# Kernel tuning notes

Measured on AMD Instinct MI355X. Metric: run time of the kernel, lower is better.

## Reference

```python
import jax, jax.numpy as jnp
import numpy as np

B, T, H, F = 32, 2048, 1024, 1024  # batch, kv_len, hidden_size, feature_size


def setup_inputs() -> dict:
    key = jax.random.key(0)
    ks = jax.random.split(key, 6)
    s = 0.02  # param init scale
    return {
        "query": jax.random.normal(ks[0], (B, 1, H), jnp.float32),
        "keys": jax.random.normal(ks[1], (B, T, F), jnp.float32),
        "Wa_w": jax.random.normal(ks[2], (H, H), jnp.float32) * s,
        "Wa_b": jnp.zeros((H,), jnp.float32),
        "Ua_w": jax.random.normal(ks[3], (H, F), jnp.float32) * s,
        "Ua_b": jnp.zeros((H,), jnp.float32),
        "Va_w": jax.random.normal(ks[4], (1, H), jnp.float32) * s,
        "Va_b": jnp.zeros((1,), jnp.float32),
    }


def reference(query, keys, Wa_w, Wa_b, Ua_w, Ua_b, Va_w, Va_b):
    # Wa(query): [B,1,H]; Ua(keys): [B,T,H]
    q = jnp.einsum('bqh,oh->bqo', query, Wa_w) + Wa_b
    k = jnp.einsum('btf,of->bto', keys, Ua_w) + Ua_b
    e = jnp.tanh(q + k)                                   # [B,T,H] (broadcast over q dim of size 1)
    scores = jnp.einsum('bth,h->bt', e, Va_w[0]) + Va_b[0]  # Va(...).squeeze(2) -> [B,T]
    scores = scores[:, None, :]                           # unsqueeze(1) -> [B,1,T]
    weights = jax.nn.softmax(scores, axis=-1)             # [B,1,T]
    context = jnp.einsum('bqt,btf->bqf', weights, keys)   # bmm -> [B,1,F]
    return context, weights
```

## Files before the change

### kernel.cpp

```cpp
#include <hip/hip_runtime.h>
#include <hip/hip_bf16.h>

typedef float  f32x4 __attribute__((ext_vector_type(4)));
typedef short  s16x8 __attribute__((ext_vector_type(8)));
typedef __hip_bfloat16 bf16;

#define BDIM 32
#define TDIM 2048
#define HDIM 1024
#define FDIM 1024
#define MTOT (BDIM*TDIM)

#define GLOAD16(gp, lp) __builtin_amdgcn_global_load_lds(                     \
    (const __attribute__((address_space(1))) void*)(gp),                      \
    (__attribute__((address_space(3))) void*)(lp), 16, 0, 0)

__global__ __launch_bounds__(256) void cvt_bf16_kernel(
    const float* __restrict__ src, bf16* __restrict__ dst, int n8)
{
    int i = blockIdx.x * 256 + threadIdx.x;
    const int stride = gridDim.x * 256;
    for (; i < n8; i += stride) {
        const f32x4 a = ((const f32x4*)src)[2 * i];
        const f32x4 b = ((const f32x4*)src)[2 * i + 1];
        union { bf16 h[8]; s16x8 v; } u;
        #pragma unroll
        for (int j = 0; j < 4; ++j) {
            u.h[j]     = __float2bfloat16(a[j]);
            u.h[4 + j] = __float2bfloat16(b[j]);
        }
        ((s16x8*)dst)[i] = u.v;
    }
}

__global__ __launch_bounds__(256) void qeff_kernel(
    const float* __restrict__ query, const float* __restrict__ Wa_w,
    const float* __restrict__ Wa_b,  const float* __restrict__ Ua_b,
    float* __restrict__ qe)
{
    const int lane = threadIdx.x & 63;
    const int gw   = blockIdx.x * 4 + (threadIdx.x >> 6);
    const int b    = gw >> 10;
    const int o    = gw & 1023;
    const float* qp = query + (size_t)b * HDIM;
    const float* wp = Wa_w  + (size_t)o * HDIM;
    float s = 0.f;
    #pragma unroll
    for (int i = 0; i < 16; ++i) {
        const int h = i * 64 + lane;
        s += qp[h] * wp[h];
    }
    #pragma unroll
    for (int off = 32; off > 0; off >>= 1) s += __shfl_down(s, off);
    if (lane == 0) qe[gw] = s + Wa_b[o] + Ua_b[o];
}

#define STAGE_A(buf_, kb_, h_, s_) GLOAD16(                                    \
    Ab + (size_t)(M0 + (h_)*128 + (((s_)>>1)<<4) + srow) * FDIM               \
       + (kb_) + (((s_)&1)<<5) + scg*8,                                        \
    &As[buf_][((((h_)*8 + ((s_)>>1)) * 2 + ((s_)&1)) << 9)])
#define STAGE_B(buf_, kb_, h_, s_) GLOAD16(                                    \
    Bb + (size_t)(N0 + (h_)*128 + (((s_)>>1)<<4) + srow) * FDIM               \
       + (kb_) + (((s_)&1)<<5) + scg*8,                                        \
    &Bs[buf_][((((h_)*8 + ((s_)>>1)) * 2 + ((s_)&1)) << 9)])

__global__ __launch_bounds__(512, 2) void score_gemm_256_kernel(
    const bf16* __restrict__ Ab, const bf16* __restrict__ Bb,
    const float* __restrict__ qe, const float* __restrict__ Va,
    float* __restrict__ scores)
{
    __shared__ bf16 As[2][16384];
    __shared__ bf16 Bs[2][16384];

    const int tid  = threadIdx.x;
    const int lane = tid & 63;
    const int w    = tid >> 6;
    const int wr   = w >> 2;
    const int wc   = w & 3;

    const int bid   = blockIdx.x;
    const int local = bid >> 3;
    const int mt    = (bid & 7) * 32 + (local >> 2);
    const int nt    = local & 3;
    const int M0 = mt * 256, N0 = nt * 256;

    const int srow = lane >> 2;
    const int scg  = (lane & 3) ^ ((lane >> 4) & 3);
    const int r    = lane & 15;
    const int roff = r * 32 + (((lane >> 4) ^ ((r >> 2) & 3)) & 3) * 8;

    f32x4 acc[8][4];
    #pragma unroll
    for (int m = 0; m < 8; ++m)
        #pragma unroll
        for (int n = 0; n < 4; ++n) acc[m][n] = (f32x4){0.f, 0.f, 0.f, 0.f};

    STAGE_A(0, 0, 0, w); STAGE_A(0, 0, 0, w + 8);
    STAGE_A(0, 0, 1, w); STAGE_A(0, 0, 1, w + 8);
    STAGE_B(0, 0, 0, w); STAGE_B(0, 0, 0, w + 8);
    STAGE_B(0, 0, 1, w); STAGE_B(0, 0, 1, w + 8);
    asm volatile("s_waitcnt vmcnt(0)" ::: "memory");
    __builtin_amdgcn_s_barrier();

    for (int t = 0; t < 16; ++t) {
        const int rb  = t & 1, wbuf = rb ^ 1;
        const int kt1 = (t + 1) << 6;
        const bool pf = (t + 1 < 16);

        s16x8 a[4][2];
        s16x8 bq[4][2];

        #pragma unroll
        for (int mf = 0; mf < 4; ++mf)
            #pragma unroll
            for (int ks = 0; ks < 2; ++ks)
                a[mf][ks] = *(const s16x8*)
                    &As[rb][(((wr * 8 + mf) * 2 + ks) << 9) + roff];
        #pragma unroll
        for (int nf = 0; nf < 2; ++nf)
            #pragma unroll
            for (int ks = 0; ks < 2; ++ks)
                bq[nf][ks] = *(const s16x8*)
                    &Bs[rb][(((wc * 4 + nf) * 2 + ks) << 9) + roff];
        if (pf) {
            STAGE_A(wbuf, kt1, 0, w); STAGE_A(wbuf, kt1, 0, w + 8);
            STAGE_A(wbuf, kt1, 1, w); STAGE_A(wbuf, kt1, 1, w + 8);
        }
        __builtin_amdgcn_s_barrier();
        __builtin_amdgcn_s_setprio(1);
        #pragma unroll
        for (int mf = 0; mf < 4; ++mf)
            #pragma unroll
            for (int nf = 0; nf < 2; ++nf)
                #pragma unroll
                for (int ks = 0; ks < 2; ++ks)
                    acc[mf][nf] = __builtin_amdgcn_mfma_f32_16x16x32_bf16(
                        a[mf][ks], bq[nf][ks], acc[mf][nf], 0, 0, 0);
        __builtin_amdgcn_s_setprio(0);
        __builtin_amdgcn_s_barrier();

        #pragma unroll
        for (int nf = 2; nf < 4; ++nf)
            #pragma unroll
            for (int ks = 0; ks < 2; ++ks)
                bq[nf][ks] = *(const s16x8*)
                    &Bs[rb][(((wc * 4 + nf) * 2 + ks) << 9) + roff];
        if (pf) {
            STAGE_B(wbuf, kt1, 0, w); STAGE_B(wbuf, kt1, 0, w + 8);
            STAGE_B(wbuf, kt1, 1, w); STAGE_B(wbuf, kt1, 1, w + 8);
        }
        __builtin_amdgcn_s_barrier();
        __builtin_amdgcn_s_setprio(1);
        #pragma unroll
        for (int mf = 0; mf < 4; ++mf)
            #pragma unroll
            for (int nf = 2; nf < 4; ++nf)
                #pragma unroll
                for (int ks = 0; ks < 2; ++ks)
                    acc[mf][nf] = __builtin_amdgcn_mfma_f32_16x16x32_bf16(
                        a[mf][ks], bq[nf][ks], acc[mf][nf], 0, 0, 0);
        __builtin_amdgcn_s_setprio(0);
        __builtin_amdgcn_s_barrier();

        #pragma unroll
        for (int mf = 0; mf < 4; ++mf)
            #pragma unroll
            for (int ks = 0; ks < 2; ++ks)
                a[mf][ks] = *(const s16x8*)
                    &As[rb][(((wr * 8 + 4 + mf) * 2 + ks) << 9) + roff];
        __builtin_amdgcn_s_barrier();
        __builtin_amdgcn_s_setprio(1);
        #pragma unroll
        for (int mf = 0; mf < 4; ++mf)
            #pragma unroll
            for (int nf = 2; nf < 4; ++nf)
                #pragma unroll
                for (int ks = 0; ks < 2; ++ks)
                    acc[4 + mf][nf] = __builtin_amdgcn_mfma_f32_16x16x32_bf16(
                        a[mf][ks], bq[nf][ks], acc[4 + mf][nf], 0, 0, 0);
        __builtin_amdgcn_s_setprio(0);
        __builtin_amdgcn_s_barrier();

        __builtin_amdgcn_s_setprio(1);
        #pragma unroll
        for (int mf = 0; mf < 4; ++mf)
            #pragma unroll
            for (int nf = 0; nf < 2; ++nf)
                #pragma unroll
                for (int ks = 0; ks < 2; ++ks)
                    acc[4 + mf][nf] = __builtin_amdgcn_mfma_f32_16x16x32_bf16(
                        a[mf][ks], bq[nf][ks], acc[4 + mf][nf], 0, 0, 0);
        __builtin_amdgcn_s_setprio(0);
        asm volatile("s_waitcnt vmcnt(0)" ::: "memory");
        __builtin_amdgcn_s_barrier();
        __builtin_amdgcn_sched_barrier(0);
    }

    const int b = M0 >> 11;
    const float* qrow = qe + (size_t)b * HDIM;
    #pragma unroll
    for (int mf = 0; mf < 8; ++mf) {
        float part[4] = {0.f, 0.f, 0.f, 0.f};
        #pragma unroll
        for (int nf = 0; nf < 4; ++nf) {
            const int c    = N0 + wc * 64 + nf * 16 + (lane & 15);
            const float va = Va[c];
            const float qv = qrow[c];
            #pragma unroll
            for (int j = 0; j < 4; ++j) {
                const float x = qv + acc[mf][nf][j];
                const float e = __expf(2.0f * x);
                part[j] += va * (1.0f - 2.0f / (e + 1.0f));
            }
        }
        #pragma unroll
        for (int j = 0; j < 4; ++j)
            #pragma unroll
            for (int off = 1; off < 16; off <<= 1)
                part[j] += __shfl_xor(part[j], off);
        if ((lane & 15) == 0) {
            const int rr = M0 + wr * 128 + mf * 16 + (lane >> 4) * 4;
            #pragma unroll
            for (int j = 0; j < 4; ++j) atomicAdd(&scores[rr + j], part[j]);
        }
    }
}

__global__ __launch_bounds__(256) void score_gemm_f32_kernel(
    const float* __restrict__ keys, const float* __restrict__ Ua,
    const float* __restrict__ qe,   const float* __restrict__ Va,
    float* __restrict__ scores)
{
    __shared__ bf16 Asf[128][40];
    __shared__ bf16 Bsf[128][40];

    const int tid  = threadIdx.x;
    const int lane = tid & 63;
    const int wid  = tid >> 6;
    const int wr   = wid >> 1, wc = wid & 1;
    const int n0   = blockIdx.x * 128;
    const int m0   = blockIdx.y * 128;

    const int srow  = tid >> 1;
    const int shalf = tid & 1;
    const float* gA = keys + (size_t)(m0 + srow) * FDIM + shalf * 16;
    const float* gB = Ua   + (size_t)(n0 + srow) * FDIM + shalf * 16;

    f32x4 acc[4][4];
    #pragma unroll
    for (int m = 0; m < 4; ++m)
        #pragma unroll
        for (int n = 0; n < 4; ++n) acc[m][n] = (f32x4){0.f, 0.f, 0.f, 0.f};

    float4 ra[4], rbv[4];
    #pragma unroll
    for (int i = 0; i < 4; ++i) {
        ra[i]  = ((const float4*)gA)[i];
        rbv[i] = ((const float4*)gB)[i];
    }

    for (int kt = 0; kt < 32; ++kt) {
        __syncthreads();
        {
            union { bf16 h[16]; s16x8 v[2]; } ua, ub;
            #pragma unroll
            for (int i = 0; i < 4; ++i) {
                const float* fa = (const float*)&ra[i];
                const float* fb = (const float*)&rbv[i];
                #pragma unroll
                for (int j = 0; j < 4; ++j) {
                    ua.h[i*4+j] = __float2bfloat16(fa[j]);
                    ub.h[i*4+j] = __float2bfloat16(fb[j]);
                }
            }
            *(s16x8*)&Asf[srow][shalf*16]     = ua.v[0];
            *(s16x8*)&Asf[srow][shalf*16 + 8] = ua.v[1];
            *(s16x8*)&Bsf[srow][shalf*16]     = ub.v[0];
            *(s16x8*)&Bsf[srow][shalf*16 + 8] = ub.v[1];
        }
        __syncthreads();

        if (kt + 1 < 32) {
            const float* pa = gA + (kt + 1) * 32;
            const float* pb = gB + (kt + 1) * 32;
            #pragma unroll
            for (int i = 0; i < 4; ++i) {
                ra[i]  = ((const float4*)pa)[i];
                rbv[i] = ((const float4*)pb)[i];
            }
        }

        s16x8 af[4], bfr[4];
        #pragma unroll
        for (int m = 0; m < 4; ++m)
            af[m] = *(const s16x8*)&Asf[wr*64 + m*16 + (lane & 15)][(lane >> 4) * 8];
        #pragma unroll
        for (int n = 0; n < 4; ++n)
            bfr[n] = *(const s16x8*)&Bsf[wc*64 + n*16 + (lane & 15)][(lane >> 4) * 8];
        #pragma unroll
        for (int m = 0; m < 4; ++m)
            #pragma unroll
            for (int n = 0; n < 4; ++n)
                acc[m][n] = __builtin_amdgcn_mfma_f32_16x16x32_bf16(
                    af[m], bfr[n], acc[m][n], 0, 0, 0);
    }

    const int b = m0 >> 11;
    const float* qrow = qe + (size_t)b * HDIM;
    #pragma unroll
    for (int m = 0; m < 4; ++m) {
        float part[4] = {0.f, 0.f, 0.f, 0.f};
        #pragma unroll
        for (int n = 0; n < 4; ++n) {
            const int c    = n0 + wc*64 + n*16 + (lane & 15);
            const float va = Va[c];
            const float qv = qrow[c];
            #pragma unroll
            for (int j = 0; j < 4; ++j) {
                const float x = qv + acc[m][n][j];
                const float e = __expf(2.0f * x);
                part[j] += va * (1.0f - 2.0f / (e + 1.0f));
            }
        }
        #pragma unroll
        for (int j = 0; j < 4; ++j)
            #pragma unroll
            for (int off = 1; off < 16; off <<= 1)
                part[j] += __shfl_xor(part[j], off);
        if ((lane & 15) == 0) {
            const int rr = m0 + wr*64 + m*16 + (lane >> 4) * 4;
            #pragma unroll
            for (int j = 0; j < 4; ++j) atomicAdd(&scores[rr + j], part[j]);
        }
    }
}

__global__ __launch_bounds__(256) void softmax_kernel(float* __restrict__ sw)
{
    const int b    = blockIdx.x;
    const int tid  = threadIdx.x;
    const int lane = tid & 63, wid = tid >> 6;
    __shared__ float red[8];

    float v[8];
    float m = -3.4e38f;
    #pragma unroll
    for (int i = 0; i < 8; ++i) {
        v[i] = sw[b * TDIM + i * 256 + tid];
        m = fmaxf(m, v[i]);
    }
    #pragma unroll
    for (int off = 32; off > 0; off >>= 1) m = fmaxf(m, __shfl_xor(m, off));
    if (lane == 0) red[wid] = m;
    __syncthreads();
    m = fmaxf(fmaxf(red[0], red[1]), fmaxf(red[2], red[3]));

    float s = 0.f;
    #pragma unroll
    for (int i = 0; i < 8; ++i) { v[i] = __expf(v[i] - m); s += v[i]; }
    #pragma unroll
    for (int off = 32; off > 0; off >>= 1) s += __shfl_xor(s, off);
    if (lane == 0) red[4 + wid] = s;
    __syncthreads();
    s = (red[4] + red[5]) + (red[6] + red[7]);

    const float inv = 1.0f / s;
    #pragma unroll
    for (int i = 0; i < 8; ++i) sw[b * TDIM + i * 256 + tid] = v[i] * inv;
}

__global__ __launch_bounds__(256) void context_bf16_kernel(
    const bf16* __restrict__ keys, const float* __restrict__ w,
    float* __restrict__ ctx)
{
    const int tc  = blockIdx.x;
    const int b   = blockIdx.y;
    const int tid = threadIdx.x;
    __shared__ float ws_[128];
    if (tid < 128) ws_[tid] = w[b * TDIM + tc * 128 + tid];
    __syncthreads();

    const bf16* kp = keys + ((size_t)b * TDIM + (size_t)tc * 128) * FDIM + tid * 4;
    float4 acc = {0.f, 0.f, 0.f, 0.f};
    #pragma unroll 8
    for (int t = 0; t < 128; ++t) {
        const short4 kv = *(const short4*)(kp + (size_t)t * FDIM);
        const float wt = ws_[t];
        acc.x += wt * __uint_as_float(((unsigned)(unsigned short)kv.x) << 16);
        acc.y += wt * __uint_as_float(((unsigned)(unsigned short)kv.y) << 16);
        acc.z += wt * __uint_as_float(((unsigned)(unsigned short)kv.z) << 16);
        acc.w += wt * __uint_as_float(((unsigned)(unsigned short)kv.w) << 16);
    }
    float* cp = ctx + (size_t)b * FDIM + tid * 4;
    atomicAdd(cp + 0, acc.x); atomicAdd(cp + 1, acc.y);
    atomicAdd(cp + 2, acc.z); atomicAdd(cp + 3, acc.w);
}

__global__ __launch_bounds__(256) void context_f32_kernel(
    const float* __restrict__ keys, const float* __restrict__ w,
    float* __restrict__ ctx)
{
    const int tc  = blockIdx.x;
    const int b   = blockIdx.y;
    const int tid = threadIdx.x;
    __shared__ float ws_[128];
    if (tid < 128) ws_[tid] = w[b * TDIM + tc * 128 + tid];
    __syncthreads();

    const float* kp = keys + ((size_t)b * TDIM + (size_t)tc * 128) * FDIM + tid * 4;
    float4 acc = {0.f, 0.f, 0.f, 0.f};
    #pragma unroll 8
    for (int t = 0; t < 128; ++t) {
        const float4 kv = *(const float4*)(kp + (size_t)t * FDIM);
        const float wt = ws_[t];
        acc.x += wt * kv.x; acc.y += wt * kv.y;
        acc.z += wt * kv.z; acc.w += wt * kv.w;
    }
    float* cp = ctx + (size_t)b * FDIM + tid * 4;
    atomicAdd(cp + 0, acc.x); atomicAdd(cp + 1, acc.y);
    atomicAdd(cp + 2, acc.z); atomicAdd(cp + 3, acc.w);
}

extern "C" void kernel_launch(void* const* d_in, const int* in_sizes, int n_in,
                              void* d_out, int out_size, void* d_ws, size_t ws_size,
                              hipStream_t stream)
{
    const float* query = (const float*)d_in[0];
    const float* keys  = (const float*)d_in[1];
    const float* Wa_w  = (const float*)d_in[2];
    const float* Wa_b  = (const float*)d_in[3];
    const float* Ua_w  = (const float*)d_in[4];
    const float* Ua_b  = (const float*)d_in[5];
    const float* Va_w  = (const float*)d_in[6];

    float* out = (float*)d_out;
    float* ctx = out;
    float* sw  = out + BDIM * HDIM;

    const size_t needA = (size_t)MTOT * FDIM * sizeof(bf16);
    const size_t needB = (size_t)HDIM * FDIM * sizeof(bf16);
    const bool fast = ws_size >= needA + needB;

    hipMemsetAsync(sw, 0, (size_t)BDIM * TDIM * sizeof(float), stream);
    qeff_kernel<<<dim3(BDIM * HDIM / 4), 256, 0, stream>>>(query, Wa_w, Wa_b, Ua_b, ctx);

    if (fast) {
        bf16* Ab = (bf16*)d_ws;
        bf16* Bb = Ab + (size_t)MTOT * FDIM;
        cvt_bf16_kernel<<<dim3(2048), 256, 0, stream>>>(keys, Ab, MTOT * FDIM / 8);
        cvt_bf16_kernel<<<dim3(512),  256, 0, stream>>>(Ua_w, Bb, HDIM * FDIM / 8);
        score_gemm_256_kernel<<<dim3(1024), 512, 0, stream>>>(Ab, Bb, ctx, Va_w, sw);
        softmax_kernel<<<dim3(BDIM), 256, 0, stream>>>(sw);
        hipMemsetAsync(ctx, 0, (size_t)BDIM * HDIM * sizeof(float), stream);
        context_bf16_kernel<<<dim3(16, BDIM), 256, 0, stream>>>(Ab, sw, ctx);
    } else {
        score_gemm_f32_kernel<<<dim3(HDIM / 128, MTOT / 128), 256, 0, stream>>>(
            keys, Ua_w, ctx, Va_w, sw);
        softmax_kernel<<<dim3(BDIM), 256, 0, stream>>>(sw);
        hipMemsetAsync(ctx, 0, (size_t)BDIM * HDIM * sizeof(float), stream);
        context_f32_kernel<<<dim3(16, BDIM), 256, 0, stream>>>(keys, sw, ctx);
    }
}
```

Baseline: 285.8 us.

## Prefetch two K-tiles ahead with partial vmcnt waits and new LDS swizzle

Restructures the score GEMM main loop to process two K-tiles per iteration over fixed LDS buffers. It primes both buffers up front and waits with vmcnt(8) so one tile's global-to-LDS loads stay in flight while the other is computed, instead of draining all loads every step. It also reorders the quadrant MFMA sequence so A fragments are reused across both N halves, changes the XOR swizzle for LDS staging and reads, and drops the 2-block occupancy hint from launch bounds. The deeper overlap aims to hide global-load latency, at the risk of more register pressure and lower occupancy.

```diff
diff --git a/kernel.cpp b/kernel.cpp
--- a/kernel.cpp
+++ b/kernel.cpp
@@ -14,6 +14,8 @@
 #define GLOAD16(gp, lp) __builtin_amdgcn_global_load_lds(                     \
     (const __attribute__((address_space(1))) void*)(gp),                      \
     (__attribute__((address_space(3))) void*)(lp), 16, 0, 0)
+
+#define MFMA_BF16 __builtin_amdgcn_mfma_f32_16x16x32_bf16
 
 __global__ __launch_bounds__(256) void cvt_bf16_kernel(
     const float* __restrict__ src, bf16* __restrict__ dst, int n8)
@@ -64,7 +66,7 @@
        + (kb_) + (((s_)&1)<<5) + scg*8,                                        \
     &Bs[buf_][((((h_)*8 + ((s_)>>1)) * 2 + ((s_)&1)) << 9)])
 
-__global__ __launch_bounds__(512, 2) void score_gemm_256_kernel(
+__global__ __launch_bounds__(512) void score_gemm_256_kernel(
     const bf16* __restrict__ Ab, const bf16* __restrict__ Bb,
     const float* __restrict__ qe, const float* __restrict__ Va,
     float* __restrict__ scores)
@@ -85,9 +87,10 @@
     const int M0 = mt * 256, N0 = nt * 256;
 
     const int srow = lane >> 2;
-    const int scg  = (lane & 3) ^ ((lane >> 4) & 3);
+    const int scg  = (lane & 3) ^ (((lane >> 5) & 1) << 1);
     const int r    = lane & 15;
-    const int roff = r * 32 + (((lane >> 4) ^ ((r >> 2) & 3)) & 3) * 8;
+    const int q4   = lane >> 4;
+    const int roff = r * 32 + ((q4 ^ (((r >> 3) & 1) << 1)) & 3) * 8;
 
     f32x4 acc[8][4];
     #pragma unroll
@@ -95,105 +98,194 @@
         #pragma unroll
         for (int n = 0; n < 4; ++n) acc[m][n] = (f32x4){0.f, 0.f, 0.f, 0.f};
 
+    STAGE_B(0, 0, 0, w); STAGE_B(0, 0, 0, w + 8);
+    STAGE_B(0, 0, 1, w); STAGE_B(0, 0, 1, w + 8);
     STAGE_A(0, 0, 0, w); STAGE_A(0, 0, 0, w + 8);
     STAGE_A(0, 0, 1, w); STAGE_A(0, 0, 1, w + 8);
-    STAGE_B(0, 0, 0, w); STAGE_B(0, 0, 0, w + 8);
-    STAGE_B(0, 0, 1, w); STAGE_B(0, 0, 1, w + 8);
-    asm volatile("s_waitcnt vmcnt(0)" ::: "memory");
+    STAGE_B(1, 64, 0, w); STAGE_B(1, 64, 0, w + 8);
+    STAGE_B(1, 64, 1, w); STAGE_B(1, 64, 1, w + 8);
+    STAGE_A(1, 64, 0, w); STAGE_A(1, 64, 0, w + 8);
+    STAGE_A(1, 64, 1, w); STAGE_A(1, 64, 1, w + 8);
+    asm volatile("s_waitcnt vmcnt(8)" ::: "memory");
     __builtin_amdgcn_s_barrier();
 
-    for (int t = 0; t < 16; ++t) {
-        const int rb  = t & 1, wbuf = rb ^ 1;
-        const int kt1 = (t + 1) << 6;
-        const bool pf = (t + 1 < 16);
-
-        s16x8 a[4][2];
-        s16x8 bq[4][2];
-
-        #pragma unroll
-        for (int mf = 0; mf < 4; ++mf)
-            #pragma unroll
-            for (int ks = 0; ks < 2; ++ks)
-                a[mf][ks] = *(const s16x8*)
-                    &As[rb][(((wr * 8 + mf) * 2 + ks) << 9) + roff];
+    for (int i = 0; i < 8; ++i) {
+        const bool pf  = (i < 7);
+        const int kbe = (2 * i + 2) << 6;
+        const int kbo = (2 * i + 3) << 6;
+
+        s16x8 a0[4][2], a1[4][2], b0[2][2], b1[2][2];
+
+        #pragma unroll
+        for (int mf = 0; mf < 4; ++mf)
+            #pragma unroll
+            for (int ks = 0; ks < 2; ++ks)
+                a0[mf][ks] = *(const s16x8*)
+                    &As[0][(((wr * 8 + mf) * 2 + ks) << 9) + roff];
         #pragma unroll
         for (int nf = 0; nf < 2; ++nf)
             #pragma unroll
             for (int ks = 0; ks < 2; ++ks)
-                bq[nf][ks] = *(const s16x8*)
-                    &Bs[rb][(((wc * 4 + nf) * 2 + ks) << 9) + roff];
+                b0[nf][ks] = *(const s16x8*)
+                    &Bs[0][(((wc * 4 + nf) * 2 + ks) << 9) + roff];
+        __builtin_amdgcn_s_barrier();
+        __builtin_amdgcn_s_setprio(1);
+        #pragma unroll
+        for (int mf = 0; mf < 4; ++mf)
+            #pragma unroll
+            for (int nf = 0; nf < 2; ++nf)
+                #pragma unroll
+                for (int ks = 0; ks < 2; ++ks)
+                    acc[mf][nf] = MFMA_BF16(a0[mf][ks], b0[nf][ks],
+                                            acc[mf][nf], 0, 0, 0);
+        __builtin_amdgcn_s_setprio(0);
+        __builtin_amdgcn_s_barrier();
+
+        #pragma unroll
+        for (int nf = 0; nf < 2; ++nf)
+            #pragma unroll
+            for (int ks = 0; ks < 2; ++ks)
+                b1[nf][ks] = *(const s16x8*)
+                    &Bs[0][(((wc * 4 + 2 + nf) * 2 + ks) << 9) + roff];
+        __builtin_amdgcn_s_barrier();
+        __builtin_amdgcn_s_setprio(1);
+        #pragma unroll
+        for (int mf = 0; mf < 4; ++mf)
+            #pragma unroll
+            for (int nf = 0; nf < 2; ++nf)
+                #pragma unroll
+                for (int ks = 0; ks < 2; ++ks)
+                    acc[mf][2 + nf] = MFMA_BF16(a0[mf][ks], b1[nf][ks],
+                                                acc[mf][2 + nf], 0, 0, 0);
+        __builtin_amdgcn_s_setprio(0);
+        __builtin_amdgcn_s_barrier();
+
+        #pragma unroll
+        for (int mf = 0; mf < 4; ++mf)
+            #pragma unroll
+            for (int ks = 0; ks < 2; ++ks)
+                a1[mf][ks] = *(const s16x8*)
+                    &As[0][(((wr * 8 + 4 + mf) * 2 + ks) << 9) + roff];
         if (pf) {
-            STAGE_A(wbuf, kt1, 0, w); STAGE_A(wbuf, kt1, 0, w + 8);
-            STAGE_A(wbuf, kt1, 1, w); STAGE_A(wbuf, kt1, 1, w + 8);
-        }
-        __builtin_amdgcn_s_barrier();
-        __builtin_amdgcn_s_setprio(1);
-        #pragma unroll
-        for (int mf = 0; mf < 4; ++mf)
-            #pragma unroll
-            for (int nf = 0; nf < 2; ++nf)
-                #pragma unroll
-                for (int ks = 0; ks < 2; ++ks)
-                    acc[mf][nf] = __builtin_amdgcn_mfma_f32_16x16x32_bf16(
-                        a[mf][ks], bq[nf][ks], acc[mf][nf], 0, 0, 0);
-        __builtin_amdgcn_s_setprio(0);
-        __builtin_amdgcn_s_barrier();
-
-        #pragma unroll
-        for (int nf = 2; nf < 4; ++nf)
-            #pragma unroll
-            for (int ks = 0; ks < 2; ++ks)
-                bq[nf][ks] = *(const s16x8*)
-                    &Bs[rb][(((wc * 4 + nf) * 2 + ks) << 9) + roff];
+            STAGE_B(0, kbe, 0, w); STAGE_B(0, kbe, 0, w + 8);
+            STAGE_B(0, kbe, 1, w); STAGE_B(0, kbe, 1, w + 8);
+        }
+        __builtin_amdgcn_s_barrier();
+        __builtin_amdgcn_s_setprio(1);
+        #pragma unroll
+        for (int mf = 0; mf < 4; ++mf)
+            #pragma unroll
+            for (int nf = 0; nf < 2; ++nf)
+                #pragma unroll
+                for (int ks = 0; ks < 2; ++ks)
+                    acc[4 + mf][nf] = MFMA_BF16(a1[mf][ks], b0[nf][ks],
+                                                acc[4 + mf][nf], 0, 0, 0);
+        __builtin_amdgcn_s_setprio(0);
+        __builtin_amdgcn_s_barrier();
+
         if (pf) {
-            STAGE_B(wbuf, kt1, 0, w); STAGE_B(wbuf, kt1, 0, w + 8);
-            STAGE_B(wbuf, kt1, 1, w); STAGE_B(wbuf, kt1, 1, w + 8);
-        }
-        __builtin_amdgcn_s_barrier();
-        __builtin_amdgcn_s_setprio(1);
-        #pragma unroll
-        for (int mf = 0; mf < 4; ++mf)
-            #pragma unroll
-            for (int nf = 2; nf < 4; ++nf)
-                #pragma unroll
-                for (int ks = 0; ks < 2; ++ks)
-                    acc[mf][nf] = __builtin_amdgcn_mfma_f32_16x16x32_bf16(
-                        a[mf][ks], bq[nf][ks], acc[mf][nf], 0, 0, 0);
-        __builtin_amdgcn_s_setprio(0);
-        __builtin_amdgcn_s_barrier();
-
-        #pragma unroll
-        for (int mf = 0; mf < 4; ++mf)
-            #pragma unroll
-            for (int ks = 0; ks < 2; ++ks)
-                a[mf][ks] = *(const s16x8*)
-                    &As[rb][(((wr * 8 + 4 + mf) * 2 + ks) << 9) + roff];
-        __builtin_amdgcn_s_barrier();
-        __builtin_amdgcn_s_setprio(1);
-        #pragma unroll
-        for (int mf = 0; mf < 4; ++mf)
-            #pragma unroll
-            for (int nf = 2; nf < 4; ++nf)
-                #pragma unroll
-                for (int ks = 0; ks < 2; ++ks)
-                    acc[4 + mf][nf] = __builtin_amdgcn_mfma_f32_16x16x32_bf16(
-                        a[mf][ks], bq[nf][ks], acc[4 + mf][nf], 0, 0, 0);
-        __builtin_amdgcn_s_setprio(0);
-        __builtin_amdgcn_s_barrier();
-
-        __builtin_amdgcn_s_setprio(1);
-        #pragma unroll
-        for (int mf = 0; mf < 4; ++mf)
-            #pragma unroll
-            for (int nf = 0; nf < 2; ++nf)
-                #pragma unroll
-                for (int ks = 0; ks < 2; ++ks)
-                    acc[4 + mf][nf] = __builtin_amdgcn_mfma_f32_16x16x32_bf16(
-                        a[mf][ks], bq[nf][ks], acc[4 + mf][nf], 0, 0, 0);
-        __builtin_amdgcn_s_setprio(0);
-        asm volatile("s_waitcnt vmcnt(0)" ::: "memory");
-        __builtin_amdgcn_s_barrier();
-        __builtin_amdgcn_sched_barrier(0);
+            STAGE_A(0, kbe, 0, w); STAGE_A(0, kbe, 0, w + 8);
+            STAGE_A(0, kbe, 1, w); STAGE_A(0, kbe, 1, w + 8);
+        }
+        __builtin_amdgcn_s_barrier();
+        __builtin_amdgcn_s_setprio(1);
+        #pragma unroll
+        for (int mf = 0; mf < 4; ++mf)
+            #pragma unroll
+            for (int nf = 0; nf < 2; ++nf)
+                #pragma unroll
+                for (int ks = 0; ks < 2; ++ks)
+                    acc[4 + mf][2 + nf] = MFMA_BF16(a1[mf][ks], b1[nf][ks],
+                                                    acc[4 + mf][2 + nf], 0, 0, 0);
+        __builtin_amdgcn_s_setprio(0);
+        if (pf) asm volatile("s_waitcnt vmcnt(8)" ::: "memory");
+        else    asm volatile("s_waitcnt vmcnt(0)" ::: "memory");
+        __builtin_amdgcn_s_barrier();
+
+        #pragma unroll
+        for (int mf = 0; mf < 4; ++mf)
+            #pragma unroll
+            for (int ks = 0; ks < 2; ++ks)
+                a0[mf][ks] = *(const s16x8*)
+                    &As[1][(((wr * 8 + mf) * 2 + ks) << 9) + roff];
+        #pragma unroll
+        for (int nf = 0; nf < 2; ++nf)
+            #pragma unroll
+            for (int ks = 0; ks < 2; ++ks)
+                b0[nf][ks] = *(const s16x8*)
+                    &Bs[1][(((wc * 4 + nf) * 2 + ks) << 9) + roff];
+        __builtin_amdgcn_s_barrier();
+        __builtin_amdgcn_s_setprio(1);
+        #pragma unroll
+        for (int mf = 0; mf < 4; ++mf)
+            #pragma unroll
+            for (int nf = 0; nf < 2; ++nf)
+                #pragma unroll
+                for (int ks = 0; ks < 2; ++ks)
+                    acc[mf][nf] = MFMA_BF16(a0[mf][ks], b0[nf][ks],
+                                            acc[mf][nf], 0, 0, 0);
+        __builtin_amdgcn_s_setprio(0);
+        __builtin_amdgcn_s_barrier();
+
+        #pragma unroll
+        for (int nf = 0; nf < 2; ++nf)
+            #pragma unroll
+            for (int ks = 0; ks < 2; ++ks)
+                b1[nf][ks] = *(const s16x8*)
+                    &Bs[1][(((wc * 4 + 2 + nf) * 2 + ks) << 9) + roff];
+        __builtin_amdgcn_s_barrier();
+        __builtin_amdgcn_s_setprio(1);
+        #pragma unroll
+        for (int mf = 0; mf < 4; ++mf)
+            #pragma unroll
+            for (int nf = 0; nf < 2; ++nf)
+                #pragma unroll
+                for (int ks = 0; ks < 2; ++ks)
+                    acc[mf][2 + nf] = MFMA_BF16(a0[mf][ks], b1[nf][ks],
+                                                acc[mf][2 + nf], 0, 0, 0);
+        __builtin_amdgcn_s_setprio(0);
+        __builtin_amdgcn_s_barrier();
+
+        #pragma unroll
+        for (int mf = 0; mf < 4; ++mf)
+            #pragma unroll
+            for (int ks = 0; ks < 2; ++ks)
+                a1[mf][ks] = *(const s16x8*)
+                    &As[1][(((wr * 8 + 4 + mf) * 2 + ks) << 9) + roff];
+        if (pf) {
+            STAGE_B(1, kbo, 0, w); STAGE_B(1, kbo, 0, w + 8);
+            STAGE_B(1, kbo, 1, w); STAGE_B(1, kbo, 1, w + 8);
+        }
+        __builtin_amdgcn_s_barrier();
+        __builtin_amdgcn_s_setprio(1);
+        #pragma unroll
+        for (int mf = 0; mf < 4; ++mf)
+            #pragma unroll
+            for (int nf = 0; nf < 2; ++nf)
+                #pragma unroll
+                for (int ks = 0; ks < 2; ++ks)
+                    acc[4 + mf][nf] = MFMA_BF16(a1[mf][ks], b0[nf][ks],
+                                                acc[4 + mf][nf], 0, 0, 0);
+        __builtin_amdgcn_s_setprio(0);
+        __builtin_amdgcn_s_barrier();
+
+        if (pf) {
+            STAGE_A(1, kbo, 0, w); STAGE_A(1, kbo, 0, w + 8);
+            STAGE_A(1, kbo, 1, w); STAGE_A(1, kbo, 1, w + 8);
+        }
+        __builtin_amdgcn_s_barrier();
+        __builtin_amdgcn_s_setprio(1);
+        #pragma unroll
+        for (int mf = 0; mf < 4; ++mf)
+            #pragma unroll
+            for (int nf = 0; nf < 2; ++nf)
+                #pragma unroll
+                for (int ks = 0; ks < 2; ++ks)
+                    acc[4 + mf][2 + nf] = MFMA_BF16(a1[mf][ks], b1[nf][ks],
+                                                    acc[4 + mf][2 + nf], 0, 0, 0);
+        __builtin_amdgcn_s_setprio(0);
+        if (pf) asm volatile("s_waitcnt vmcnt(8)" ::: "memory");
+        __builtin_amdgcn_s_barrier();
     }
 
     const int b = M0 >> 11;
@@ -301,8 +393,7 @@
         for (int m = 0; m < 4; ++m)
             #pragma unroll
             for (int n = 0; n < 4; ++n)
-                acc[m][n] = __builtin_amdgcn_mfma_f32_16x16x32_bf16(
-                    af[m], bfr[n], acc[m][n], 0, 0, 0);
+                acc[m][n] = MFMA_BF16(af[m], bfr[n], acc[m][n], 0, 0, 0);
     }
 
     const int b = m0 >> 11;
```

New measurement: 277.2 us. 3.0% less time.

## Prefetch two k-tiles ahead with vmcnt-based waits and simplified LDS swizzle

Applied to the files above, without the earlier changes.

Restructures the main GEMM loop so the first two k-tiles are staged up front and each iteration issues loads two tiles ahead into the buffer just consumed. The next tile is gated by a partial vmcnt wait instead of a full drain. Each iteration now loads all A and B fragments at once and splits the MFMAs into two halves around a single barrier, replacing the previous four-phase schedule with many barriers. The LDS swizzle pattern also changes. This aims to hide global-load latency and cut barrier overhead, at the cost of higher register pressure from holding 8x2 A fragments and some risk in the vmcnt counting.

```diff
diff --git a/kernel.cpp b/kernel.cpp
--- a/kernel.cpp
+++ b/kernel.cpp
@@ -14,6 +14,8 @@
 #define GLOAD16(gp, lp) __builtin_amdgcn_global_load_lds(                     \
     (const __attribute__((address_space(1))) void*)(gp),                      \
     (__attribute__((address_space(3))) void*)(lp), 16, 0, 0)
+
+#define MFMA_BF16 __builtin_amdgcn_mfma_f32_16x16x32_bf16
 
 __global__ __launch_bounds__(256) void cvt_bf16_kernel(
     const float* __restrict__ src, bf16* __restrict__ dst, int n8)
@@ -85,9 +87,10 @@
     const int M0 = mt * 256, N0 = nt * 256;
 
     const int srow = lane >> 2;
-    const int scg  = (lane & 3) ^ ((lane >> 4) & 3);
+    const int scg  = (lane & 3) ^ (((lane >> 5) & 1) << 1);
     const int r    = lane & 15;
-    const int roff = r * 32 + (((lane >> 4) ^ ((r >> 2) & 3)) & 3) * 8;
+    const int q4   = lane >> 4;
+    const int roff = r * 32 + ((q4 ^ (((r >> 3) & 1) << 1)) & 3) * 8;
 
     f32x4 acc[8][4];
     #pragma unroll
@@ -95,105 +98,78 @@
         #pragma unroll
         for (int n = 0; n < 4; ++n) acc[m][n] = (f32x4){0.f, 0.f, 0.f, 0.f};
 
+    STAGE_B(0, 0, 0, w); STAGE_B(0, 0, 0, w + 8);
+    STAGE_B(0, 0, 1, w); STAGE_B(0, 0, 1, w + 8);
     STAGE_A(0, 0, 0, w); STAGE_A(0, 0, 0, w + 8);
     STAGE_A(0, 0, 1, w); STAGE_A(0, 0, 1, w + 8);
-    STAGE_B(0, 0, 0, w); STAGE_B(0, 0, 0, w + 8);
-    STAGE_B(0, 0, 1, w); STAGE_B(0, 0, 1, w + 8);
-    asm volatile("s_waitcnt vmcnt(0)" ::: "memory");
+    STAGE_B(1, 64, 0, w); STAGE_B(1, 64, 0, w + 8);
+    STAGE_B(1, 64, 1, w); STAGE_B(1, 64, 1, w + 8);
+    STAGE_A(1, 64, 0, w); STAGE_A(1, 64, 0, w + 8);
+    STAGE_A(1, 64, 1, w); STAGE_A(1, 64, 1, w + 8);
+    asm volatile("s_waitcnt vmcnt(8)" ::: "memory");
     __builtin_amdgcn_s_barrier();
 
+    #pragma unroll 2
     for (int t = 0; t < 16; ++t) {
-        const int rb  = t & 1, wbuf = rb ^ 1;
-        const int kt1 = (t + 1) << 6;
-        const bool pf = (t + 1 < 16);
-
-        s16x8 a[4][2];
-        s16x8 bq[4][2];
-
-        #pragma unroll
-        for (int mf = 0; mf < 4; ++mf)
+        const int p = t & 1;
+        s16x8 a[8][2], b[4][2];
+
+        #pragma unroll
+        for (int mf = 0; mf < 8; ++mf)
             #pragma unroll
             for (int ks = 0; ks < 2; ++ks)
                 a[mf][ks] = *(const s16x8*)
-                    &As[rb][(((wr * 8 + mf) * 2 + ks) << 9) + roff];
-        #pragma unroll
-        for (int nf = 0; nf < 2; ++nf)
+                    &As[p][(((wr * 8 + mf) * 2 + ks) << 9) + roff];
+        #pragma unroll
+        for (int nf = 0; nf < 4; ++nf)
             #pragma unroll
             for (int ks = 0; ks < 2; ++ks)
-                bq[nf][ks] = *(const s16x8*)
-                    &Bs[rb][(((wc * 4 + nf) * 2 + ks) << 9) + roff];
-        if (pf) {
-            STAGE_A(wbuf, kt1, 0, w); STAGE_A(wbuf, kt1, 0, w + 8);
-            STAGE_A(wbuf, kt1, 1, w); STAGE_A(wbuf, kt1, 1, w + 8);
-        }
-        __builtin_amdgcn_s_barrier();
+                b[nf][ks] = *(const s16x8*)
+                    &Bs[p][(((wc * 4 + nf) * 2 + ks) << 9) + roff];
+
         __builtin_amdgcn_s_setprio(1);
         #pragma unroll
         for (int mf = 0; mf < 4; ++mf)
             #pragma unroll
-            for (int nf = 0; nf < 2; ++nf)
+            for (int nf = 0; nf < 4; ++nf)
                 #pragma unroll
                 for (int ks = 0; ks < 2; ++ks)
-                    acc[mf][nf] = __builtin_amdgcn_mfma_f32_16x16x32_bf16(
-                        a[mf][ks], bq[nf][ks], acc[mf][nf], 0, 0, 0);
+                    acc[mf][nf] = MFMA_BF16(a[mf][ks], b[nf][ks],
+                                            acc[mf][nf], 0, 0, 0);
         __builtin_amdgcn_s_setprio(0);
+
+        asm volatile("s_waitcnt lgkmcnt(0)" ::: "memory");
         __builtin_amdgcn_s_barrier();
-
-        #pragma unroll
-        for (int nf = 2; nf < 4; ++nf)
-            #pragma unroll
-            for (int ks = 0; ks < 2; ++ks)
-                bq[nf][ks] = *(const s16x8*)
-                    &Bs[rb][(((wc * 4 + nf) * 2 + ks) << 9) + roff];
-        if (pf) {
-            STAGE_B(wbuf, kt1, 0, w); STAGE_B(wbuf, kt1, 0, w + 8);
-            STAGE_B(wbuf, kt1, 1, w); STAGE_B(wbuf, kt1, 1, w + 8);
-        }
-        __builtin_amdgcn_s_barrier();
+        __builtin_amdgcn_sched_barrier(0);
+
+        if (t + 2 < 16) {
+            const int kb = (t + 2) << 6;
+            STAGE_B(p, kb, 0, w); STAGE_B(p, kb, 0, w + 8);
+            STAGE_B(p, kb, 1, w); STAGE_B(p, kb, 1, w + 8);
+            STAGE_A(p, kb, 0, w); STAGE_A(p, kb, 0, w + 8);
+            STAGE_A(p, kb, 1, w); STAGE_A(p, kb, 1, w + 8);
+        }
+
         __builtin_amdgcn_s_setprio(1);
         #pragma unroll
-        for (int mf = 0; mf < 4; ++mf)
-            #pragma unroll
-            for (int nf = 2; nf < 4; ++nf)
+        for (int mf = 4; mf < 8; ++mf)
+            #pragma unroll
+            for (int nf = 0; nf < 4; ++nf)
                 #pragma unroll
                 for (int ks = 0; ks < 2; ++ks)
-                    acc[mf][nf] = __builtin_amdgcn_mfma_f32_16x16x32_bf16(
-                        a[mf][ks], bq[nf][ks], acc[mf][nf], 0, 0, 0);
+                    acc[mf][nf] = MFMA_BF16(a[mf][ks], b[nf][ks],
+                                            acc[mf][nf], 0, 0, 0);
         __builtin_amdgcn_s_setprio(0);
-        __builtin_amdgcn_s_barrier();
-
-        #pragma unroll
-        for (int mf = 0; mf < 4; ++mf)
-            #pragma unroll
-            for (int ks = 0; ks < 2; ++ks)
-                a[mf][ks] = *(const s16x8*)
-                    &As[rb][(((wr * 8 + 4 + mf) * 2 + ks) << 9) + roff];
-        __builtin_amdgcn_s_barrier();
-        __builtin_amdgcn_s_setprio(1);
-        #pragma unroll
-        for (int mf = 0; mf < 4; ++mf)
-            #pragma unroll
-            for (int nf = 2; nf < 4; ++nf)
-                #pragma unroll
-                for (int ks = 0; ks < 2; ++ks)
-                    acc[4 + mf][nf] = __builtin_amdgcn_mfma_f32_16x16x32_bf16(
-                        a[mf][ks], bq[nf][ks], acc[4 + mf][nf], 0, 0, 0);
-        __builtin_amdgcn_s_setprio(0);
-        __builtin_amdgcn_s_barrier();
-
-        __builtin_amdgcn_s_setprio(1);
-        #pragma unroll
-        for (int mf = 0; mf < 4; ++mf)
-            #pragma unroll
-            for (int nf = 0; nf < 2; ++nf)
-                #pragma unroll
-                for (int ks = 0; ks < 2; ++ks)
-                    acc[4 + mf][nf] = __builtin_amdgcn_mfma_f32_16x16x32_bf16(
-                        a[mf][ks], bq[nf][ks], acc[4 + mf][nf], 0, 0, 0);
-        __builtin_amdgcn_s_setprio(0);
-        asm volatile("s_waitcnt vmcnt(0)" ::: "memory");
-        __builtin_amdgcn_s_barrier();
-        __builtin_amdgcn_sched_barrier(0);
+
+        if (t < 14) {
+            asm volatile("s_waitcnt vmcnt(8)" ::: "memory");
+            __builtin_amdgcn_s_barrier();
+            __builtin_amdgcn_sched_barrier(0);
+        } else if (t == 14) {
+            asm volatile("s_waitcnt vmcnt(0)" ::: "memory");
+            __builtin_amdgcn_s_barrier();
+            __builtin_amdgcn_sched_barrier(0);
+        }
     }
 
     const int b = M0 >> 11;
@@ -301,8 +277,7 @@
         for (int m = 0; m < 4; ++m)
             #pragma unroll
             for (int n = 0; n < 4; ++n)
-                acc[m][n] = __builtin_amdgcn_mfma_f32_16x16x32_bf16(
-                    af[m], bfr[n], acc[m][n], 0, 0, 0);
+                acc[m][n] = MFMA_BF16(af[m], bfr[n], acc[m][n], 0, 0, 0);
     }
 
     const int b = m0 >> 11;
```

Result: slower. 338.2 us (+18.3%).
